# Kernel optimization log

Measured on AMD Instinct MI355X. Metric: run time of the kernel, lower is better.

The kernel has to match this reference:

```python
import jax, jax.numpy as jnp
import numpy as np

B, N = 16, 512            # graphs, atoms per graph
F_DIM, H, D = 128, 64, 16  # feature_dim, hidden_dim, far_source_dim
CUT, GROWTH = 5.0, 2.0
NS, NT = 3, 2
MULT = GROWTH ** NS        # default far_max_radius_multiplier = 8
EMAX = CUT * MULT          # 40.0
TOT = NS + NT              # 5 shells total
SF = D + 3                 # 19 per-shell features
SE_IN = TOT * SF           # 95
EH_IN = 4 * D + SE_IN      # 159
N_RBF = 8
BOUNDS = [(5.0, 10.0), (10.0, 20.0), (20.0, 40.0), (40.0, 80.0), (80.0, float('inf'))]


def ln(x, g, b):
    m = x.mean(-1, keepdims=True)
    v = x.var(-1, keepdims=True)
    return (x - m) / jnp.sqrt(v + 1e-5) * g + b


def setup_inputs() -> dict:
    key = jax.random.key(0)
    ks = jax.random.split(key, 16)
    W = lambda k, i, o: jax.random.normal(k, (i, o), jnp.float32) / np.sqrt(i)
    inp = {}
    inp['x'] = jax.random.normal(ks[0], (B * N, F_DIM), jnp.float32)
    inp['pos'] = jax.random.uniform(ks[1], (B * N, 3), jnp.float32) * 80.0
    inp['batch'] = jnp.repeat(jnp.arange(B, dtype=jnp.int32), N)
    inp['num_graphs'] = B
    inp['in_ln_g'] = jnp.ones(F_DIM); inp['in_ln_b'] = jnp.zeros(F_DIM)
    inp['src_w1'] = W(ks[2], F_DIM, H); inp['src_b1'] = jnp.zeros(H)
    inp['src_w2'] = W(ks[3], H, D);     inp['src_b2'] = jnp.zeros(D)
    inp['src_ln_g'] = jnp.ones(D); inp['src_ln_b'] = jnp.zeros(D)
    inp['se_ln_g'] = jnp.ones(SE_IN); inp['se_ln_b'] = jnp.zeros(SE_IN)
    inp['se_w1'] = W(ks[4], SE_IN, H); inp['se_b1'] = jnp.zeros(H)
    inp['se_w2'] = W(ks[5], H, D);     inp['se_b2'] = jnp.zeros(D)
    inp['eh_ln_g'] = jnp.ones(EH_IN); inp['eh_ln_b'] = jnp.zeros(EH_IN)
    inp['eh_w1'] = W(ks[6], EH_IN, H); inp['eh_b1'] = jnp.zeros(H)
    inp['eh_w2'] = W(ks[7], H, 1);     inp['eh_b2'] = jnp.zeros(1)
    inp['k_screen'] = jnp.float32(-8.0)
    inp['kg_w1'] = W(ks[8], N_RBF + 2, 32); inp['kg_b1'] = jnp.zeros(32)
    inp['kg_w2'] = jnp.zeros((32, 1)); inp['kg_b2'] = jnp.zeros(1)  # zero-init per source
    inp['far_gate'] = jnp.float32(0.2)
    inp['energy_scale'] = jnp.float32(0.0)
    return inp


def reference(x, pos, batch, num_graphs, in_ln_g, in_ln_b, src_w1, src_b1, src_w2, src_b2,
              src_ln_g, src_ln_b, se_ln_g, se_ln_b, se_w1, se_b1, se_w2, se_b2,
              eh_ln_g, eh_ln_b, eh_w1, eh_b1, eh_w2, eh_b2,
              k_screen, kg_w1, kg_b1, kg_w2, kg_b2, far_gate, energy_scale):
    M = x.shape[0]
    n = M // num_graphs
    # per-atom source features
    h = ln(x, in_ln_g, in_ln_b)
    src = jax.nn.silu(h @ src_w1 + src_b1) @ src_w2 + src_b2
    src = ln(src, src_ln_g, src_ln_b)
    # graph-wise neutralization (subtract per-graph mean)
    gsum = jax.ops.segment_sum(src, batch, num_segments=num_graphs)
    cnt = jax.ops.segment_sum(jnp.ones((M, 1), x.dtype), batch, num_segments=num_graphs)
    src = src - (gsum / jnp.maximum(cnt, 1.0))[batch]
    # pairwise distances per graph
    p = pos.reshape(num_graphs, n, 3)
    s = src.reshape(num_graphs, n, D)
    diff = p[:, :, None, :] - p[:, None, :, :]
    d = jnp.sqrt((diff * diff).sum(-1) + 1e-12)  # [B,n,n]
    not_self = ~jnp.eye(n, dtype=bool)[None]
    # physical kernel with learned RBF gate
    screening = jax.nn.softplus(k_screen)
    base = jnp.exp(-screening * d) / jnp.maximum(d, 1e-6)
    centers = jnp.linspace(CUT, EMAX, N_RBF)
    spacing = (EMAX - CUT) / (N_RBF - 1)
    gamma = 1.0 / (spacing * spacing)
    dc = d[..., None]
    rbf = jnp.exp(-gamma * (dc - centers) ** 2)
    gin = jnp.concatenate([dc / CUT, dc / EMAX, rbf], -1)
    gate = 1.0 + jnp.tanh(jax.nn.silu(gin @ kg_w1 + kg_b1) @ kg_w2 + kg_b2)[..., 0]
    ker = base * gate
    # shell statistics: kernel-weighted mean source, count, mean_r, rms_r per shell
    feats = []
    for lo, up in BOUNDS:
        m = (d >= lo) & not_self
        if np.isfinite(up):
            m = m & (d < up)
        mf = m.astype(x.dtype)
        c = mf.sum(-1)
        denom = jnp.maximum(c, 1.0)
        mean = jnp.einsum('bij,bjc->bic', ker * mf, s) / denom[..., None]
        mr = (mf * d).sum(-1) / denom
        rr = jnp.sqrt((mf * d * d).sum(-1) / denom + 1e-12)
        feats.append(jnp.concatenate([mean, c[..., None], mr[..., None], rr[..., None]], -1))
    shell = jnp.concatenate(feats, -1).reshape(M, SE_IN)  # [M, 95]
    emb = jax.nn.silu(ln(shell, se_ln_g, se_ln_b) @ se_w1 + se_b1) @ se_w2 + se_b2
    ein = jnp.concatenate([src, emb, src * emb, src - emb, shell], -1)  # [M, 159]
    pa = (jax.nn.silu(ln(ein, eh_ln_g, eh_ln_b) @ eh_w1 + eh_b1) @ eh_w2 + eh_b2)[..., 0]
    pa = pa * jnp.tanh(far_gate) * jnp.exp(energy_scale)
    return jax.ops.segment_sum(pa, batch, num_segments=num_graphs)  # per-graph energies [B]
```

## Files before the change

kernel.cpp:

```cpp
#include <hip/hip_runtime.h>
#include <math.h>

#define B_G   16
#define N_A   512
#define M_AT  8192
#define FD    128
#define HD    64
#define DD    16
#define SEIN  95
#define EHIN  159
#define NLUT  512
#define DMAXF 140.0f
#define NFB   512

__device__ __forceinline__ float silu_f(float z) { return z / (1.f + __expf(-z)); }

__global__ __launch_bounds__(256) void k_front(
    const float* __restrict__ x,
    const float* __restrict__ g, const float* __restrict__ bb,
    const float* __restrict__ w1, const float* __restrict__ b1,
    const float* __restrict__ w2, const float* __restrict__ b2,
    const float* __restrict__ lng, const float* __restrict__ lnb,
    const float* __restrict__ k_screen,
    const float* __restrict__ kg_w1, const float* __restrict__ kg_b1,
    const float* __restrict__ kg_w2, const float* __restrict__ kg_b2,
    float* __restrict__ srcout, float* __restrict__ partials,
    float2* __restrict__ lut, float* __restrict__ out) {
  int t = threadIdx.x;

  if (blockIdx.x >= NFB) {
    int lb = blockIdx.x - NFB;
    __shared__ float w1l[320], b1l[32], w2l[32];
    if (lb == 0 && t < B_G) out[t] = 0.f;
    for (int idx = t; idx < 320; idx += 256) w1l[idx] = kg_w1[idx];
    if (t < 32) { b1l[t] = kg_b1[t]; w2l[t] = kg_w2[t]; }
    __syncthreads();
    int i = lb * 256 + t;
    float step = DMAXF / (float)(NLUT - 1);
    float ksv = k_screen[0];
    float screening = fmaxf(ksv, 0.f) + log1pf(expf(-fabsf(ksv)));
    float b2v = kg_b2[0];
    float vals[2];
#pragma unroll
    for (int e = 0; e < 2; ++e) {
      int ii = min(i + e, NLUT - 1);
      float d = (float)ii * step;
      float base = expf(-screening * d) / fmaxf(d, 1e-6f);
      float gin[10];
      gin[0] = d * (1.f / 5.0f);
      gin[1] = d * (1.f / 40.0f);
#pragma unroll
      for (int kk = 0; kk < 8; ++kk) {
        float u = d - (5.0f + 5.0f * (float)kk);
        gin[2 + kk] = expf(-(1.f / 25.f) * u * u);
      }
      float accv = 0.f;
      for (int h = 0; h < 32; ++h) {
        float z = b1l[h];
#pragma unroll
        for (int kk = 0; kk < 10; ++kk) z += gin[kk] * w1l[kk * 32 + h];
        accv += silu_f(z) * w2l[h];
      }
      vals[e] = base * (1.f + tanhf(accv + b2v));
    }
    lut[i] = make_float2(vals[0], vals[1] - vals[0]);
    return;
  }

  int wave = t >> 6, lane = t & 63;
  int ag = lane >> 4, l16 = lane & 15;
  int a = wave * 4 + ag;
  int atom = blockIdx.x * 16 + a;

  __shared__ __align__(16) float xn[16 * 132];
  __shared__ __align__(16) float hb[16 * 68];
  __shared__ float psum[4][16];

  float xr[8];
  {
    const float4* xp = (const float4*)(x + (size_t)atom * FD + l16 * 8);
    float4 v0 = xp[0], v1 = xp[1];
    xr[0] = v0.x; xr[1] = v0.y; xr[2] = v0.z; xr[3] = v0.w;
    xr[4] = v1.x; xr[5] = v1.y; xr[6] = v1.z; xr[7] = v1.w;
  }
  float s = 0.f;
#pragma unroll
  for (int i = 0; i < 8; ++i) s += xr[i];
  s += __shfl_xor(s, 1); s += __shfl_xor(s, 2); s += __shfl_xor(s, 4); s += __shfl_xor(s, 8);
  float m = s * (1.f / 128.f);
  float v2 = 0.f;
#pragma unroll
  for (int i = 0; i < 8; ++i) { float d = xr[i] - m; v2 += d * d; }
  v2 += __shfl_xor(v2, 1); v2 += __shfl_xor(v2, 2); v2 += __shfl_xor(v2, 4); v2 += __shfl_xor(v2, 8);
  float inv = rsqrtf(v2 * (1.f / 128.f) + 1e-5f);
  {
    int kb = l16 * 8;
    float4 gv0 = ((const float4*)g)[l16 * 2], gv1 = ((const float4*)g)[l16 * 2 + 1];
    float4 bv0 = ((const float4*)bb)[l16 * 2], bv1 = ((const float4*)bb)[l16 * 2 + 1];
    float4 o0, o1;
    o0.x = (xr[0] - m) * inv * gv0.x + bv0.x;
    o0.y = (xr[1] - m) * inv * gv0.y + bv0.y;
    o0.z = (xr[2] - m) * inv * gv0.z + bv0.z;
    o0.w = (xr[3] - m) * inv * gv0.w + bv0.w;
    o1.x = (xr[4] - m) * inv * gv1.x + bv1.x;
    o1.y = (xr[5] - m) * inv * gv1.y + bv1.y;
    o1.z = (xr[6] - m) * inv * gv1.z + bv1.z;
    o1.w = (xr[7] - m) * inv * gv1.w + bv1.w;
    *(float4*)&xn[a * 132 + kb] = o0;
    *(float4*)&xn[a * 132 + kb + 4] = o1;
  }
  __syncthreads();

  float acc[4] = {0.f, 0.f, 0.f, 0.f};
  {
    const float* xnb = &xn[a * 132];
#pragma unroll 4
    for (int k = 0; k < FD; k += 4) {
      float4 xa = *(const float4*)(xnb + k);
      float4 wa = ((const float4*)(w1 + (size_t)(k + 0) * HD))[l16];
      float4 wbv = ((const float4*)(w1 + (size_t)(k + 1) * HD))[l16];
      float4 wc = ((const float4*)(w1 + (size_t)(k + 2) * HD))[l16];
      float4 wd = ((const float4*)(w1 + (size_t)(k + 3) * HD))[l16];
      acc[0] += wa.x * xa.x; acc[0] += wbv.x * xa.y; acc[0] += wc.x * xa.z; acc[0] += wd.x * xa.w;
      acc[1] += wa.y * xa.x; acc[1] += wbv.y * xa.y; acc[1] += wc.y * xa.z; acc[1] += wd.y * xa.w;
      acc[2] += wa.z * xa.x; acc[2] += wbv.z * xa.y; acc[2] += wc.z * xa.z; acc[2] += wd.z * xa.w;
      acc[3] += wa.w * xa.x; acc[3] += wbv.w * xa.y; acc[3] += wc.w * xa.z; acc[3] += wd.w * xa.w;
    }
    float4 bv = ((const float4*)b1)[l16];
    float4 ho;
    ho.x = silu_f(acc[0] + bv.x); ho.y = silu_f(acc[1] + bv.y);
    ho.z = silu_f(acc[2] + bv.z); ho.w = silu_f(acc[3] + bv.w);
    *(float4*)&hb[a * 68 + l16 * 4] = ho;
  }
  __syncthreads();

  {
    float acc2 = 0.f;
    const float* hbb = &hb[a * 68];
#pragma unroll
    for (int h = 0; h < HD; h += 4) {
      float4 hv = *(const float4*)(hbb + h);
      acc2 += w2[(h + 0) * DD + l16] * hv.x;
      acc2 += w2[(h + 1) * DD + l16] * hv.y;
      acc2 += w2[(h + 2) * DD + l16] * hv.z;
      acc2 += w2[(h + 3) * DD + l16] * hv.w;
    }
    float val = acc2 + b2[l16];
    float sm = val;
    sm += __shfl_xor(sm, 1); sm += __shfl_xor(sm, 2); sm += __shfl_xor(sm, 4); sm += __shfl_xor(sm, 8);
    float mm = sm * (1.f / 16.f);
    float dv = val - mm;
    float vv = dv * dv;
    vv += __shfl_xor(vv, 1); vv += __shfl_xor(vv, 2); vv += __shfl_xor(vv, 4); vv += __shfl_xor(vv, 8);
    float iv = rsqrtf(vv * (1.f / 16.f) + 1e-5f);
    float ov = dv * iv * lng[l16] + lnb[l16];
    srcout[(size_t)atom * DD + l16] = ov;
    float lsum = ov;
    lsum += __shfl_xor(lsum, 16); lsum += __shfl_xor(lsum, 32);
    if (lane < 16) psum[wave][l16] = lsum;
  }
  __syncthreads();
  if (t < 16)
    partials[(size_t)blockIdx.x * 16 + t] =
        psum[0][t] + psum[1][t] + psum[2][t] + psum[3][t];
}

__global__ __launch_bounds__(256) void k_pairs(
    const float* __restrict__ pos, const float* __restrict__ src,
    const float2* __restrict__ lut, const float* __restrict__ partials,
    float* __restrict__ shell) {
  int gph = blockIdx.x >> 7;
  int blk = blockIdx.x & 127;
  int t = threadIdx.x, wave = t >> 6, lane = t & 63;
  int i_local = blk * 4 + wave;

  __shared__ __align__(16) float2 luts[NLUT];
  __shared__ __align__(16) unsigned wb[4][N_A];
  __shared__ float smean[16];

  const float* posg = pos + (size_t)gph * N_A * 3;
  const float* srcg = src + (size_t)gph * N_A * DD;

  if (t < NLUT / 2) ((float4*)luts)[t] = ((const float4*)lut)[t];
  if (t < 64) {
    int c = t & 15, grp = t >> 4;
    float sm = 0.f;
#pragma unroll
    for (int k = 0; k < 8; ++k)
      sm += partials[(size_t)(gph * 32 + grp * 8 + k) * 16 + c];
    sm += __shfl_xor(sm, 16); sm += __shfl_xor(sm, 32);
    if (t < 16) smean[c] = sm * (1.f / 512.f);
  }

  float px = posg[i_local * 3], py = posg[i_local * 3 + 1], pz = posg[i_local * 3 + 2];
  __syncthreads();

  float cnt[5] = {0,0,0,0,0}, sd[5] = {0,0,0,0,0}, sdd[5] = {0,0,0,0,0}, sw[5] = {0,0,0,0,0};
  const float lscale = (float)(NLUT - 1) / DMAXF;

#pragma unroll
  for (int it = 0; it < 8; ++it) {
    int jv = lane + it * 64;
    float qx = posg[jv * 3], qy = posg[jv * 3 + 1], qz = posg[jv * 3 + 2];
    float dx = px - qx, dy = py - qy, dz = pz - qz;
    float d2 = dx * dx + dy * dy + dz * dz + 1e-12f;
    float d = sqrtf(d2);
    bool valid = (jv != i_local) && (d >= 5.0f);
    int tq = (d >= 10.f) + (d >= 20.f) + (d >= 40.f) + (d >= 80.f);
    float xq = d * lscale;
    int i0 = min((int)xq, NLUT - 2);
    float f = xq - (float)i0;
    float2 L = luts[i0];
    float w = valid ? (L.x + L.y * f) : 0.f;
    wb[wave][jv] = (__float_as_uint(w) & ~7u) | (unsigned)tq;
    float dm = valid ? d : 0.f;
    float ddm = valid ? d * d : 0.f;
    float cm = valid ? 1.f : 0.f;
#pragma unroll
    for (int q = 0; q < 5; ++q) {
      bool mq = (tq == q);
      cnt[q] += mq ? cm : 0.f;
      sd[q]  += mq ? dm : 0.f;
      sdd[q] += mq ? ddm : 0.f;
      sw[q]  += mq ? w : 0.f;
    }
  }
#pragma unroll
  for (int q = 0; q < 5; ++q) {
#pragma unroll
    for (int o = 32; o > 0; o >>= 1) {
      cnt[q] += __shfl_xor(cnt[q], o);
      sd[q]  += __shfl_xor(sd[q], o);
      sdd[q] += __shfl_xor(sdd[q], o);
      sw[q]  += __shfl_xor(sw[q], o);
    }
  }
  __syncthreads();

  int cq = lane & 3, jlow = lane >> 2;
  float accq[5][4] = {};
  const float* ssb = srcg + jlow * DD + cq * 4;
  const unsigned* wbb = &wb[wave][jlow];
#pragma unroll
  for (int jj = 0; jj < 32; ++jj) {
    float4 sv = *(const float4*)(ssb + jj * 256);
    unsigned u = wbb[jj * 16];
    int tq = (int)(u & 7u);
    float w = __uint_as_float(u & ~7u);
    float w0 = (tq == 0) ? w : 0.f;
    float w1_ = (tq == 1) ? w : 0.f;
    float w2_ = (tq == 2) ? w : 0.f;
    float w3_ = (tq == 3) ? w : 0.f;
    float w4_ = (tq == 4) ? w : 0.f;
    accq[0][0] += w0 * sv.x; accq[0][1] += w0 * sv.y; accq[0][2] += w0 * sv.z; accq[0][3] += w0 * sv.w;
    accq[1][0] += w1_ * sv.x; accq[1][1] += w1_ * sv.y; accq[1][2] += w1_ * sv.z; accq[1][3] += w1_ * sv.w;
    accq[2][0] += w2_ * sv.x; accq[2][1] += w2_ * sv.y; accq[2][2] += w2_ * sv.z; accq[2][3] += w2_ * sv.w;
    accq[3][0] += w3_ * sv.x; accq[3][1] += w3_ * sv.y; accq[3][2] += w3_ * sv.z; accq[3][3] += w3_ * sv.w;
    accq[4][0] += w4_ * sv.x; accq[4][1] += w4_ * sv.y; accq[4][2] += w4_ * sv.z; accq[4][3] += w4_ * sv.w;
  }
#pragma unroll
  for (int q = 0; q < 5; ++q)
#pragma unroll
    for (int i = 0; i < 4; ++i) {
      float v = accq[q][i];
      v += __shfl_xor(v, 4); v += __shfl_xor(v, 8); v += __shfl_xor(v, 16); v += __shfl_xor(v, 32);
      accq[q][i] = v;
    }

  float* shp = shell + (size_t)(gph * N_A + i_local) * SEIN;
  if (jlow == 0) {
#pragma unroll
    for (int q = 0; q < 5; ++q) {
      float denom = fmaxf(cnt[q], 1.f);
#pragma unroll
      for (int i = 0; i < 4; ++i) {
        int c = cq * 4 + i;
        shp[q * 19 + c] = (accq[q][i] - smean[c] * sw[q]) / denom;
      }
    }
  }
  if (lane < 5) {
    int q = lane;
    float denom = fmaxf(cnt[q], 1.f);
    shp[q * 19 + 16] = cnt[q];
    shp[q * 19 + 17] = sd[q] / denom;
    shp[q * 19 + 18] = sqrtf(sdd[q] / denom + 1e-12f);
  }
}

__global__ __launch_bounds__(256) void k_tail(
    const float* __restrict__ src, const float* __restrict__ shell,
    const float* __restrict__ partials,
    const float* __restrict__ se_ln_g, const float* __restrict__ se_ln_b,
    const float* __restrict__ se_w1, const float* __restrict__ se_b1,
    const float* __restrict__ se_w2, const float* __restrict__ se_b2,
    const float* __restrict__ eh_ln_g, const float* __restrict__ eh_ln_b,
    const float* __restrict__ eh_w1, const float* __restrict__ eh_b1,
    const float* __restrict__ eh_w2, const float* __restrict__ eh_b2,
    const float* __restrict__ far_gate, const float* __restrict__ energy_scale,
    float* __restrict__ out) {
  int t = threadIdx.x, wave = t >> 6, lane = t & 63;
  int ag = lane >> 4, l16 = lane & 15;
  int a = wave * 4 + ag;
  int aB = blockIdx.x * 16;
  int gph = aB >> 9;

  __shared__ __align__(16) float ein[16 * 160];
  __shared__ __align__(16) float shn[16 * 96];
  __shared__ __align__(16) float hb[16 * 68];
  __shared__ float smean[16];
  __shared__ float redv[4];

  if (t < 64) {
    int c = t & 15, grp = t >> 4;
    float sm = 0.f;
#pragma unroll
    for (int k = 0; k < 8; ++k)
      sm += partials[(size_t)(gph * 32 + grp * 8 + k) * 16 + c];
    sm += __shfl_xor(sm, 16); sm += __shfl_xor(sm, 32);
    if (t < 16) smean[c] = sm * (1.f / 512.f);
  }

  const float* shg = shell + (size_t)aB * SEIN;
  for (int idx = t; idx < 16 * SEIN; idx += 256) {
    unsigned a_loc = ((unsigned)idx * 690u) >> 16;
    int kk = idx - (int)a_loc * SEIN;
    ein[a_loc * 160 + 64 + kk] = shg[idx];
  }
  __syncthreads();

  {
    float s1 = 0.f, sq = 0.f;
    const float* eb = &ein[a * 160 + 64];
#pragma unroll
    for (int i = 0; i < 6; ++i) {
      int k = l16 * 6 + i;
      if (k < SEIN) { float v = eb[k]; s1 += v; sq += v * v; }
    }
    s1 += __shfl_xor(s1, 1); s1 += __shfl_xor(s1, 2); s1 += __shfl_xor(s1, 4); s1 += __shfl_xor(s1, 8);
    sq += __shfl_xor(sq, 1); sq += __shfl_xor(sq, 2); sq += __shfl_xor(sq, 4); sq += __shfl_xor(sq, 8);
    float m = s1 * (1.f / (float)SEIN);
    float var = sq * (1.f / (float)SEIN) - m * m;
    float inv = rsqrtf(var + 1e-5f);
#pragma unroll
    for (int i = 0; i < 6; ++i) {
      int k = l16 * 6 + i;
      if (k < SEIN)
        shn[a * 96 + k] = (eb[k] - m) * inv * se_ln_g[k] + se_ln_b[k];
    }
  }
  __syncthreads();

  int h0 = l16 * 4;
  {
    float acc[4] = {0.f, 0.f, 0.f, 0.f};
    const float* sb = &shn[a * 96];
#pragma unroll 4
    for (int k = 0; k < 92; k += 4) {
      float4 xa = *(const float4*)(sb + k);
      float4 wa = ((const float4*)(se_w1 + (size_t)(k + 0) * HD))[l16];
      float4 wbv = ((const float4*)(se_w1 + (size_t)(k + 1) * HD))[l16];
      float4 wc = ((const float4*)(se_w1 + (size_t)(k + 2) * HD))[l16];
      float4 wd = ((const float4*)(se_w1 + (size_t)(k + 3) * HD))[l16];
      acc[0] += wa.x * xa.x; acc[0] += wbv.x * xa.y; acc[0] += wc.x * xa.z; acc[0] += wd.x * xa.w;
      acc[1] += wa.y * xa.x; acc[1] += wbv.y * xa.y; acc[1] += wc.y * xa.z; acc[1] += wd.y * xa.w;
      acc[2] += wa.z * xa.x; acc[2] += wbv.z * xa.y; acc[2] += wc.z * xa.z; acc[2] += wd.z * xa.w;
      acc[3] += wa.w * xa.x; acc[3] += wbv.w * xa.y; acc[3] += wc.w * xa.z; acc[3] += wd.w * xa.w;
    }
#pragma unroll
    for (int k = 92; k < SEIN; ++k) {
      float xa = sb[k];
      float4 wa = ((const float4*)(se_w1 + (size_t)k * HD))[l16];
      acc[0] += wa.x * xa; acc[1] += wa.y * xa; acc[2] += wa.z * xa; acc[3] += wa.w * xa;
    }
    float4 bv = ((const float4*)se_b1)[l16];
    float4 ho;
    ho.x = silu_f(acc[0] + bv.x); ho.y = silu_f(acc[1] + bv.y);
    ho.z = silu_f(acc[2] + bv.z); ho.w = silu_f(acc[3] + bv.w);
    *(float4*)&hb[a * 68 + h0] = ho;
  }
  __syncthreads();

  {
    float acc2 = 0.f;
    const float* hbb = &hb[a * 68];
#pragma unroll
    for (int h = 0; h < HD; h += 4) {
      float4 hv = *(const float4*)(hbb + h);
      acc2 += se_w2[(h + 0) * DD + l16] * hv.x;
      acc2 += se_w2[(h + 1) * DD + l16] * hv.y;
      acc2 += se_w2[(h + 2) * DD + l16] * hv.z;
      acc2 += se_w2[(h + 3) * DD + l16] * hv.w;
    }
    float ev = acc2 + se_b2[l16];
    float sv = src[(size_t)(aB + a) * DD + l16] - smean[l16];
    ein[a * 160 + l16] = sv;
    ein[a * 160 + 16 + l16] = ev;
    ein[a * 160 + 32 + l16] = sv * ev;
    ein[a * 160 + 48 + l16] = sv - ev;
  }
  __syncthreads();

  {
    float s1 = 0.f, sq = 0.f;
    float* eb = &ein[a * 160];
#pragma unroll
    for (int i = 0; i < 10; ++i) {
      int k = l16 * 10 + i;
      if (k < EHIN) { float v = eb[k]; s1 += v; sq += v * v; }
    }
    s1 += __shfl_xor(s1, 1); s1 += __shfl_xor(s1, 2); s1 += __shfl_xor(s1, 4); s1 += __shfl_xor(s1, 8);
    sq += __shfl_xor(sq, 1); sq += __shfl_xor(sq, 2); sq += __shfl_xor(sq, 4); sq += __shfl_xor(sq, 8);
    float m = s1 * (1.f / (float)EHIN);
    float var = sq * (1.f / (float)EHIN) - m * m;
    float inv = rsqrtf(var + 1e-5f);
#pragma unroll
    for (int i = 0; i < 10; ++i) {
      int k = l16 * 10 + i;
      if (k < EHIN)
        eb[k] = (eb[k] - m) * inv * eh_ln_g[k] + eh_ln_b[k];
    }
  }
  __syncthreads();

  {
    float acc[4] = {0.f, 0.f, 0.f, 0.f};
    const float* eb = &ein[a * 160];
#pragma unroll 4
    for (int k = 0; k < 156; k += 4) {
      float4 xa = *(const float4*)(eb + k);
      float4 wa = ((const float4*)(eh_w1 + (size_t)(k + 0) * HD))[l16];
      float4 wbv = ((const float4*)(eh_w1 + (size_t)(k + 1) * HD))[l16];
      float4 wc = ((const float4*)(eh_w1 + (size_t)(k + 2) * HD))[l16];
      float4 wd = ((const float4*)(eh_w1 + (size_t)(k + 3) * HD))[l16];
      acc[0] += wa.x * xa.x; acc[0] += wbv.x * xa.y; acc[0] += wc.x * xa.z; acc[0] += wd.x * xa.w;
      acc[1] += wa.y * xa.x; acc[1] += wbv.y * xa.y; acc[1] += wc.y * xa.z; acc[1] += wd.y * xa.w;
      acc[2] += wa.z * xa.x; acc[2] += wbv.z * xa.y; acc[2] += wc.z * xa.z; acc[2] += wd.z * xa.w;
      acc[3] += wa.w * xa.x; acc[3] += wbv.w * xa.y; acc[3] += wc.w * xa.z; acc[3] += wd.w * xa.w;
    }
#pragma unroll
    for (int k = 156; k < EHIN; ++k) {
      float xa = eb[k];
      float4 wa = ((const float4*)(eh_w1 + (size_t)k * HD))[l16];
      acc[0] += wa.x * xa; acc[1] += wa.y * xa; acc[2] += wa.z * xa; acc[3] += wa.w * xa;
    }
    float4 b1v = ((const float4*)eh_b1)[l16];
    float4 w2v = ((const float4*)eh_w2)[l16];
    float pa = silu_f(acc[0] + b1v.x) * w2v.x + silu_f(acc[1] + b1v.y) * w2v.y
             + silu_f(acc[2] + b1v.z) * w2v.z + silu_f(acc[3] + b1v.w) * w2v.w;
    pa += __shfl_xor(pa, 1); pa += __shfl_xor(pa, 2); pa += __shfl_xor(pa, 4); pa += __shfl_xor(pa, 8);
    pa += __shfl_xor(pa, 16); pa += __shfl_xor(pa, 32);
    if (lane == 0) redv[wave] = pa + 4.f * eh_b2[0];
  }
  __syncthreads();
  if (t == 0) {
    float tot = redv[0] + redv[1] + redv[2] + redv[3];
    atomicAdd(&out[gph], tot * tanhf(far_gate[0]) * expf(energy_scale[0]));
  }
}

extern "C" void kernel_launch(void* const* d_in, const int* in_sizes, int n_in,
                              void* d_out, int out_size, void* d_ws, size_t ws_size,
                              hipStream_t stream) {
  const float* x         = (const float*)d_in[0];
  const float* pos       = (const float*)d_in[1];
  const float* in_ln_g   = (const float*)d_in[4];
  const float* in_ln_b   = (const float*)d_in[5];
  const float* src_w1    = (const float*)d_in[6];
  const float* src_b1    = (const float*)d_in[7];
  const float* src_w2    = (const float*)d_in[8];
  const float* src_b2    = (const float*)d_in[9];
  const float* src_ln_g  = (const float*)d_in[10];
  const float* src_ln_b  = (const float*)d_in[11];
  const float* se_ln_g   = (const float*)d_in[12];
  const float* se_ln_b   = (const float*)d_in[13];
  const float* se_w1     = (const float*)d_in[14];
  const float* se_b1     = (const float*)d_in[15];
  const float* se_w2     = (const float*)d_in[16];
  const float* se_b2     = (const float*)d_in[17];
  const float* eh_ln_g   = (const float*)d_in[18];
  const float* eh_ln_b   = (const float*)d_in[19];
  const float* eh_w1     = (const float*)d_in[20];
  const float* eh_b1     = (const float*)d_in[21];
  const float* eh_w2     = (const float*)d_in[22];
  const float* eh_b2     = (const float*)d_in[23];
  const float* k_screen  = (const float*)d_in[24];
  const float* kg_w1     = (const float*)d_in[25];
  const float* kg_b1     = (const float*)d_in[26];
  const float* kg_w2     = (const float*)d_in[27];
  const float* kg_b2     = (const float*)d_in[28];
  const float* far_gate  = (const float*)d_in[29];
  const float* en_scale  = (const float*)d_in[30];
  float* out = (float*)d_out;

  float* ws_src   = (float*)d_ws;
  float* ws_shell = ws_src + (size_t)M_AT * DD;
  float* ws_part  = ws_shell + (size_t)M_AT * SEIN;
  float2* ws_lut  = (float2*)(ws_part + NFB * 16);

  k_front<<<NFB + 2, 256, 0, stream>>>(x, in_ln_g, in_ln_b, src_w1, src_b1,
                                       src_w2, src_b2, src_ln_g, src_ln_b,
                                       k_screen, kg_w1, kg_b1, kg_w2, kg_b2,
                                       ws_src, ws_part, ws_lut, out);
  k_pairs<<<B_G * (N_A / 4), 256, 0, stream>>>(pos, ws_src, ws_lut, ws_part, ws_shell);
  k_tail<<<M_AT / 16, 256, 0, stream>>>(ws_src, ws_shell, ws_part,
                                        se_ln_g, se_ln_b, se_w1, se_b1, se_w2, se_b2,
                                        eh_ln_g, eh_ln_b, eh_w1, eh_b1, eh_w2, eh_b2,
                                        far_gate, en_scale, out);
}
```

Measured before the change: 185.7 us.

## Halve atoms per block in front kernel, assign 32 lanes per atom

The front MLP kernel now handles 8 atoms per block with 32 lanes each instead of 16 atoms with 16 lanes, doubling the block count to 1024. Each lane computes 2 hidden units instead of 4, and the second layer splits the hidden sum across two half-groups merged with a shuffle. The partial-sum layout in the downstream kernels is updated to read 64 partials per graph. The aim is more parallelism and less per-thread serial work in the front stage, at the cost of more blocks, redundant weight loads and extra partial reads.

```diff
diff --git a/kernel.cpp b/kernel.cpp
--- a/kernel.cpp
+++ b/kernel.cpp
@@ -11,7 +11,7 @@
 #define EHIN  159
 #define NLUT  512
 #define DMAXF 140.0f
-#define NFB   512
+#define NFB   1024
 
 __device__ __forceinline__ float silu_f(float z) { return z / (1.f + __expf(-z)); }
 
@@ -68,84 +68,72 @@
   }
 
   int wave = t >> 6, lane = t & 63;
-  int ag = lane >> 4, l16 = lane & 15;
-  int a = wave * 4 + ag;
-  int atom = blockIdx.x * 16 + a;
-
-  __shared__ __align__(16) float xn[16 * 132];
-  __shared__ __align__(16) float hb[16 * 68];
+  int half = lane >> 5, l32 = lane & 31;
+  int a = wave * 2 + half;
+  int atom = blockIdx.x * 8 + a;
+
+  __shared__ __align__(16) float xn[8 * 132];
+  __shared__ __align__(16) float hb[8 * 68];
   __shared__ float psum[4][16];
 
-  float xr[8];
-  {
-    const float4* xp = (const float4*)(x + (size_t)atom * FD + l16 * 8);
-    float4 v0 = xp[0], v1 = xp[1];
-    xr[0] = v0.x; xr[1] = v0.y; xr[2] = v0.z; xr[3] = v0.w;
-    xr[4] = v1.x; xr[5] = v1.y; xr[6] = v1.z; xr[7] = v1.w;
-  }
-  float s = 0.f;
-#pragma unroll
-  for (int i = 0; i < 8; ++i) s += xr[i];
-  s += __shfl_xor(s, 1); s += __shfl_xor(s, 2); s += __shfl_xor(s, 4); s += __shfl_xor(s, 8);
+  float4 xv = ((const float4*)(x + (size_t)atom * FD))[l32];
+  float s = xv.x + xv.y + xv.z + xv.w;
+  s += __shfl_xor(s, 1); s += __shfl_xor(s, 2); s += __shfl_xor(s, 4);
+  s += __shfl_xor(s, 8); s += __shfl_xor(s, 16);
   float m = s * (1.f / 128.f);
-  float v2 = 0.f;
-#pragma unroll
-  for (int i = 0; i < 8; ++i) { float d = xr[i] - m; v2 += d * d; }
-  v2 += __shfl_xor(v2, 1); v2 += __shfl_xor(v2, 2); v2 += __shfl_xor(v2, 4); v2 += __shfl_xor(v2, 8);
+  float d0 = xv.x - m, d1 = xv.y - m, d2 = xv.z - m, d3 = xv.w - m;
+  float v2 = d0 * d0 + d1 * d1 + d2 * d2 + d3 * d3;
+  v2 += __shfl_xor(v2, 1); v2 += __shfl_xor(v2, 2); v2 += __shfl_xor(v2, 4);
+  v2 += __shfl_xor(v2, 8); v2 += __shfl_xor(v2, 16);
   float inv = rsqrtf(v2 * (1.f / 128.f) + 1e-5f);
   {
-    int kb = l16 * 8;
-    float4 gv0 = ((const float4*)g)[l16 * 2], gv1 = ((const float4*)g)[l16 * 2 + 1];
-    float4 bv0 = ((const float4*)bb)[l16 * 2], bv1 = ((const float4*)bb)[l16 * 2 + 1];
-    float4 o0, o1;
-    o0.x = (xr[0] - m) * inv * gv0.x + bv0.x;
-    o0.y = (xr[1] - m) * inv * gv0.y + bv0.y;
-    o0.z = (xr[2] - m) * inv * gv0.z + bv0.z;
-    o0.w = (xr[3] - m) * inv * gv0.w + bv0.w;
-    o1.x = (xr[4] - m) * inv * gv1.x + bv1.x;
-    o1.y = (xr[5] - m) * inv * gv1.y + bv1.y;
-    o1.z = (xr[6] - m) * inv * gv1.z + bv1.z;
-    o1.w = (xr[7] - m) * inv * gv1.w + bv1.w;
-    *(float4*)&xn[a * 132 + kb] = o0;
-    *(float4*)&xn[a * 132 + kb + 4] = o1;
-  }
-  __syncthreads();
-
-  float acc[4] = {0.f, 0.f, 0.f, 0.f};
+    float4 gv = ((const float4*)g)[l32];
+    float4 bv = ((const float4*)bb)[l32];
+    float4 o;
+    o.x = d0 * inv * gv.x + bv.x;
+    o.y = d1 * inv * gv.y + bv.y;
+    o.z = d2 * inv * gv.z + bv.z;
+    o.w = d3 * inv * gv.w + bv.w;
+    *(float4*)&xn[a * 132 + l32 * 4] = o;
+  }
+  __syncthreads();
+
+  float acc0 = 0.f, acc1 = 0.f;
   {
     const float* xnb = &xn[a * 132];
 #pragma unroll 4
     for (int k = 0; k < FD; k += 4) {
       float4 xa = *(const float4*)(xnb + k);
-      float4 wa = ((const float4*)(w1 + (size_t)(k + 0) * HD))[l16];
-      float4 wbv = ((const float4*)(w1 + (size_t)(k + 1) * HD))[l16];
-      float4 wc = ((const float4*)(w1 + (size_t)(k + 2) * HD))[l16];
-      float4 wd = ((const float4*)(w1 + (size_t)(k + 3) * HD))[l16];
-      acc[0] += wa.x * xa.x; acc[0] += wbv.x * xa.y; acc[0] += wc.x * xa.z; acc[0] += wd.x * xa.w;
-      acc[1] += wa.y * xa.x; acc[1] += wbv.y * xa.y; acc[1] += wc.y * xa.z; acc[1] += wd.y * xa.w;
-      acc[2] += wa.z * xa.x; acc[2] += wbv.z * xa.y; acc[2] += wc.z * xa.z; acc[2] += wd.z * xa.w;
-      acc[3] += wa.w * xa.x; acc[3] += wbv.w * xa.y; acc[3] += wc.w * xa.z; acc[3] += wd.w * xa.w;
-    }
-    float4 bv = ((const float4*)b1)[l16];
-    float4 ho;
-    ho.x = silu_f(acc[0] + bv.x); ho.y = silu_f(acc[1] + bv.y);
-    ho.z = silu_f(acc[2] + bv.z); ho.w = silu_f(acc[3] + bv.w);
-    *(float4*)&hb[a * 68 + l16 * 4] = ho;
-  }
-  __syncthreads();
-
-  {
+      float2 wa = ((const float2*)(w1 + (size_t)(k + 0) * HD))[l32];
+      float2 wbv = ((const float2*)(w1 + (size_t)(k + 1) * HD))[l32];
+      float2 wc = ((const float2*)(w1 + (size_t)(k + 2) * HD))[l32];
+      float2 wd = ((const float2*)(w1 + (size_t)(k + 3) * HD))[l32];
+      acc0 += wa.x * xa.x; acc0 += wbv.x * xa.y; acc0 += wc.x * xa.z; acc0 += wd.x * xa.w;
+      acc1 += wa.y * xa.x; acc1 += wbv.y * xa.y; acc1 += wc.y * xa.z; acc1 += wd.y * xa.w;
+    }
+    float2 bv = ((const float2*)b1)[l32];
+    float2 ho;
+    ho.x = silu_f(acc0 + bv.x);
+    ho.y = silu_f(acc1 + bv.y);
+    *(float2*)&hb[a * 68 + l32 * 2] = ho;
+  }
+  __syncthreads();
+
+  {
+    int c = l32 & 15, hh = l32 >> 4;
     float acc2 = 0.f;
-    const float* hbb = &hb[a * 68];
-#pragma unroll
-    for (int h = 0; h < HD; h += 4) {
+    const float* hbb = &hb[a * 68 + hh * 32];
+#pragma unroll
+    for (int h = 0; h < 32; h += 4) {
       float4 hv = *(const float4*)(hbb + h);
-      acc2 += w2[(h + 0) * DD + l16] * hv.x;
-      acc2 += w2[(h + 1) * DD + l16] * hv.y;
-      acc2 += w2[(h + 2) * DD + l16] * hv.z;
-      acc2 += w2[(h + 3) * DD + l16] * hv.w;
-    }
-    float val = acc2 + b2[l16];
+      int hg = hh * 32 + h;
+      acc2 += w2[(hg + 0) * DD + c] * hv.x;
+      acc2 += w2[(hg + 1) * DD + c] * hv.y;
+      acc2 += w2[(hg + 2) * DD + c] * hv.z;
+      acc2 += w2[(hg + 3) * DD + c] * hv.w;
+    }
+    acc2 += __shfl_xor(acc2, 16);
+    float val = acc2 + b2[c];
     float sm = val;
     sm += __shfl_xor(sm, 1); sm += __shfl_xor(sm, 2); sm += __shfl_xor(sm, 4); sm += __shfl_xor(sm, 8);
     float mm = sm * (1.f / 16.f);
@@ -153,11 +141,11 @@
     float vv = dv * dv;
     vv += __shfl_xor(vv, 1); vv += __shfl_xor(vv, 2); vv += __shfl_xor(vv, 4); vv += __shfl_xor(vv, 8);
     float iv = rsqrtf(vv * (1.f / 16.f) + 1e-5f);
-    float ov = dv * iv * lng[l16] + lnb[l16];
-    srcout[(size_t)atom * DD + l16] = ov;
+    float ov = dv * iv * lng[c] + lnb[c];
+    if ((lane & 31) < 16) srcout[(size_t)atom * DD + c] = ov;
     float lsum = ov;
-    lsum += __shfl_xor(lsum, 16); lsum += __shfl_xor(lsum, 32);
-    if (lane < 16) psum[wave][l16] = lsum;
+    lsum += __shfl_xor(lsum, 32);
+    if (lane < 16) psum[wave][lane] = lsum;
   }
   __syncthreads();
   if (t < 16)
@@ -186,8 +174,8 @@
     int c = t & 15, grp = t >> 4;
     float sm = 0.f;
 #pragma unroll
-    for (int k = 0; k < 8; ++k)
-      sm += partials[(size_t)(gph * 32 + grp * 8 + k) * 16 + c];
+    for (int k = 0; k < 16; ++k)
+      sm += partials[(size_t)(gph * 64 + grp * 16 + k) * 16 + c];
     sm += __shfl_xor(sm, 16); sm += __shfl_xor(sm, 32);
     if (t < 16) smean[c] = sm * (1.f / 512.f);
   }
@@ -315,8 +303,8 @@
     int c = t & 15, grp = t >> 4;
     float sm = 0.f;
 #pragma unroll
-    for (int k = 0; k < 8; ++k)
-      sm += partials[(size_t)(gph * 32 + grp * 8 + k) * 16 + c];
+    for (int k = 0; k < 16; ++k)
+      sm += partials[(size_t)(gph * 64 + grp * 16 + k) * 16 + c];
     sm += __shfl_xor(sm, 16); sm += __shfl_xor(sm, 32);
     if (t < 16) smean[c] = sm * (1.f / 512.f);
   }
```

Measured after the change: 198.0 us. 1.07x slower.
